# Kernel tuning notes

Hardware: AMD Instinct MI355X
Metric: run time of the kernel (lower is better)

## Reference

```python
import jax, jax.numpy as jnp
import numpy as np

NU, NI = 100000, 50000          # num_users, num_items
N = NU + NI                      # total nodes
D = 64                           # hidden_dim
DE = 16                          # eigs_dim
L = 2                            # n_layers
E = 1500000                      # edges per layer
NP = 14                          # 2**(sample_hop+1)-2 path types
EPS = 1e-5


def setup_inputs() -> dict:
    key = jax.random.key(0)
    ks = jax.random.split(key, 7)
    return {
        "user_emb": jax.random.normal(ks[0], (NU, D), jnp.float32) * 0.1,
        "item_emb": jax.random.normal(ks[1], (NI, D), jnp.float32) * 0.1,
        "eigs": jax.random.normal(ks[2], (N, DE), jnp.float32),
        "lambda0": jax.random.normal(ks[3], (L,), jnp.float32) * 0.1,
        "path_w": jax.random.normal(ks[4], (L, NP), jnp.float32) * 0.1,
        "indices": jax.random.randint(ks[5], (L, 2, E), 0, N),
        "path_type": jax.random.randint(ks[6], (L, E), 0, NP),
    }


def _layer_norm(x):
    mu = x.mean(-1, keepdims=True)
    var = ((x - mu) ** 2).mean(-1, keepdims=True)
    return (x - mu) * jax.lax.rsqrt(var + EPS)


def _sparse_softmax(row, vals, n):
    # torch: clamp(exp(v), min=-5, max=5) -> effectively min(exp(v), 5)
    e = jnp.clip(jnp.exp(vals), -5.0, 5.0)
    s = jax.ops.segment_sum(e, row, num_segments=n)
    s = jnp.where(s == 0.0, 1.0, s)
    return e / s[row]


def _encoder(x, idx, pt, eigs, lam, pw):
    y = _layer_norm(x)                                   # [N, D]
    r, c = idx[0], idx[1]                                # [E]
    yc = y[c]                                            # [E, D]
    xs = (y[r] * yc).sum(-1) * (1.0 / jnp.sqrt(jnp.float32(D)))  # [E]
    ys = (eigs[r] * eigs[c]).sum(-1)                     # [E]
    s0 = _sparse_softmax(r, xs + jnp.exp(lam) * ys, N)
    s1 = _sparse_softmax(r, pw[pt], N)
    s = 0.5 * (s0 + s1)                                  # mean over the two scores
    # SpMM: out[r] += s_e * y[c_e]
    return jax.ops.segment_sum(s[:, None] * yc, r, num_segments=N)


def reference(user_emb, item_emb, eigs, lambda0, path_w, indices, path_type):
    x = jnp.concatenate([user_emb, item_emb], axis=0)    # [N, D]
    embs = [x]
    for l in range(L):
        x = _encoder(x, indices[l], path_type[l], eigs, lambda0[l], path_w[l])
        embs.append(x)
    return jnp.mean(jnp.stack(embs, axis=1), axis=1)      # [N, D]
```

## Files before the change

kernel.cpp:

```cpp
#include <hip/hip_runtime.h>
#include <hip/hip_bf16.h>

#define NUSERS 100000
#define NITEMS 50000
#define NN 150000
#define DD 64
#define DE 16
#define NE 1500000
#define NPATH 14
#define LN_EPS 1e-5f

#define BROWS 512
#define NBUK 293
#define NB (2 * NBUK)
#define CHUNK 4096
#define NCHUNK ((NE + CHUNK - 1) / CHUNK)

#define EIGBLK ((NN * DE) / 256)

typedef float vf2 __attribute__((ext_vector_type(2)));

__device__ __forceinline__ vf2 unpk(unsigned u) {
    vf2 r;
    r.x = __uint_as_float(u << 16);
    r.y = __uint_as_float(u & 0xffff0000u);
    return r;
}
__device__ __forceinline__ unsigned f2b(float f) {
    union { float f; unsigned u; } v; v.f = f;
    return (v.u + 0x7fffu + ((v.u >> 16) & 1u)) >> 16;
}

template<int CTRL>
__device__ __forceinline__ float dppmov(float x) {
    return __int_as_float(
        __builtin_amdgcn_mov_dpp(__float_as_int(x), CTRL, 0xF, 0xF, true));
}

__device__ __forceinline__ int wscan(int v, int lane) {
    #pragma unroll
    for (int d = 1; d < 64; d <<= 1) {
        int u = __shfl_up(v, d, 64);
        v += (lane >= d) ? u : 0;
    }
    return v;
}

__global__ void k_eigln(const float* __restrict__ uemb,
                        const float* __restrict__ iemb,
                        const float* __restrict__ eigs,
                        unsigned short* __restrict__ e16,
                        unsigned short* __restrict__ y) {
    int blk = blockIdx.x;
    int t = threadIdx.x;
    if (blk < EIGBLK) {
        int i = blk * 256 + t;
        e16[i] = (unsigned short)f2b(eigs[i]);
    } else {
        int row = (blk - EIGBLK) * 4 + (t >> 6);
        int lane = t & 63;
        if (row >= NN) return;
        int i = row * DD + lane;
        float v = (row < NUSERS) ? uemb[i] : iemb[i - NUSERS * DD];
        float s = v;
        #pragma unroll
        for (int m = 32; m; m >>= 1) s += __shfl_xor(s, m, 64);
        float mu = s * (1.0f / 64.0f);
        float d = v - mu;
        float q = d * d;
        #pragma unroll
        for (int m = 32; m; m >>= 1) q += __shfl_xor(q, m, 64);
        float rs = rsqrtf(q * (1.0f / 64.0f) + LN_EPS);
        y[i] = (unsigned short)f2b(d * rs);
    }
}

__global__ void k_pcount(const int* __restrict__ idx, int* __restrict__ cntmat) {
    int blk = blockIdx.x;
    int layer = blk / NCHUNK;
    int k = blk - layer * NCHUNK;
    __shared__ int h[NBUK];
    for (int t = threadIdx.x; t < NBUK; t += 256) h[t] = 0;
    __syncthreads();
    const int* rrow = idx + (size_t)layer * 2 * NE;
    int base = k * CHUNK;
    int lim = min(CHUNK, NE - base);
    for (int j = threadIdx.x; j < lim; j += 256)
        atomicAdd(&h[rrow[base + j] >> 9], 1);
    __syncthreads();
    for (int t = threadIdx.x; t < NBUK; t += 256)
        cntmat[((size_t)layer * NBUK + t) * NCHUNK + k] = h[t];
}

__global__ __launch_bounds__(512) void k_bukscan(const int* __restrict__ cnt,
                                                 int* __restrict__ exsc,
                                                 int* __restrict__ tot) {
    __shared__ int wsum[8];
    int b = blockIdx.x;
    int t = threadIdx.x;
    int lane = t & 63, w = t >> 6;
    int v = (t < NCHUNK) ? cnt[(size_t)b * NCHUNK + t] : 0;
    int s = wscan(v, lane);
    if (lane == 63) wsum[w] = s;
    __syncthreads();
    if (w == 0) {
        int x = (lane < 8) ? wsum[lane] : 0;
        #pragma unroll
        for (int d = 1; d < 8; d <<= 1) {
            int u = __shfl_up(x, d, 64);
            x += (lane >= d) ? u : 0;
        }
        if (lane < 8) wsum[lane] = x;
    }
    __syncthreads();
    int base = (w > 0) ? wsum[w - 1] : 0;
    s += base;
    if (t < NCHUNK) exsc[(size_t)b * NCHUNK + t] = s - v;
    if (t == 511) tot[b] = s;
}

__global__ __launch_bounds__(1024) void k_totscan(const int* __restrict__ tot,
                                                  int* __restrict__ bstart) {
    __shared__ int wsum[16];
    int t = threadIdx.x;
    int lane = t & 63, w = t >> 6;
    int v = (t < NB) ? tot[t] : 0;
    int s = wscan(v, lane);
    if (lane == 63) wsum[w] = s;
    __syncthreads();
    if (w == 0) {
        int x = (lane < 16) ? wsum[lane] : 0;
        #pragma unroll
        for (int d = 1; d < 16; d <<= 1) {
            int u = __shfl_up(x, d, 64);
            x += (lane >= d) ? u : 0;
        }
        if (lane < 16) wsum[lane] = x;
    }
    __syncthreads();
    int base = (w > 0) ? wsum[w - 1] : 0;
    s += base;
    if (t < NB) bstart[t] = s - v;
    if (t == 0) bstart[NB] = 2 * NE;
}

__global__ void k_pscatter(const int* __restrict__ idx,
                           const int* __restrict__ ptyp,
                           const int* __restrict__ exsc,
                           const int* __restrict__ bstart,
                           unsigned int* __restrict__ stage) {
    int blk = blockIdx.x;
    int layer = blk / NCHUNK;
    int k = blk - layer * NCHUNK;
    __shared__ int hofs[NBUK];
    for (int t = threadIdx.x; t < NBUK; t += 256) {
        int b = layer * NBUK + t;
        hofs[t] = bstart[b] + exsc[(size_t)b * NCHUNK + k];
    }
    __syncthreads();
    const int* rrow = idx + (size_t)layer * 2 * NE;
    const int* ccol = rrow + NE;
    const int* pp   = ptyp + (size_t)layer * NE;
    int base = k * CHUNK;
    int lim = min(CHUNK, NE - base);
    for (int j = threadIdx.x; j < lim; j += 256) {
        int e = base + j;
        int r = rrow[e];
        int pos = atomicAdd(&hofs[r >> 9], 1);
        stage[pos] = (unsigned)ccol[e] | ((unsigned)pp[e] << 18)
                   | ((unsigned)(r & 511) << 22);
    }
}

__global__ __launch_bounds__(1024) void k_bscatter(
        const unsigned int* __restrict__ stage,
        const int* __restrict__ bstart,
        int* __restrict__ csv,
        int2* __restrict__ roff) {
    __shared__ int scnt[BROWS];
    __shared__ int scur[BROWS];
    __shared__ int wsum[16];
    int b = blockIdx.x;
    int t = threadIdx.x;
    int lane = t & 63, w = t >> 6;
    int layer = b / NBUK;
    int brow0 = (b - layer * NBUK) * BROWS;
    int nrows = min(BROWS, NN - brow0);
    int start = bstart[b];
    int n = bstart[b + 1] - start;
    if (t < BROWS) scnt[t] = 0;
    __syncthreads();
    for (int p = t; p < n; p += 1024)
        atomicAdd(&scnt[stage[start + p] >> 22], 1);
    __syncthreads();
    int orig = (t < BROWS) ? scnt[t] : 0;
    int s = wscan(orig, lane);
    if (lane == 63) wsum[w] = s;
    __syncthreads();
    if (w == 0) {
        int x = (lane < 16) ? wsum[lane] : 0;
        #pragma unroll
        for (int d = 1; d < 16; d <<= 1) {
            int u = __shfl_up(x, d, 64);
            x += (lane >= d) ? u : 0;
        }
        if (lane < 16) wsum[lane] = x;
    }
    __syncthreads();
    int wb = (w > 0) ? wsum[w - 1] : 0;
    int excl = wb + s - orig;
    if (t < BROWS) {
        scur[t] = excl;
        if (t < nrows)
            roff[(size_t)layer * NN + brow0 + t] =
                make_int2(start + excl, start + excl + orig);
    }
    __syncthreads();
    for (int p = t; p < n; p += 1024) {
        unsigned rec = stage[start + p];
        int pos = atomicAdd(&scur[rec >> 22], 1);
        csv[start + pos] = (int)(rec & 0x3fffffu);
    }
}

__global__ void k_row(const unsigned short* __restrict__ y,
                      const unsigned short* __restrict__ e16,
                      const int2* __restrict__ roff,
                      const int* __restrict__ csv,
                      const float* __restrict__ pw,
                      const float* __restrict__ lam,
                      int layer,
                      const float* __restrict__ uemb,
                      const float* __restrict__ iemb,
                      float* __restrict__ x1,
                      unsigned short* __restrict__ y1,
                      float* __restrict__ out) {
    __shared__ float pexp[NPATH];
    __shared__ float selam;
    int t = threadIdx.x;
    if (t < NPATH) pexp[t] = fminf(expf(pw[layer * NPATH + t]), 5.0f);
    if (t == NPATH) selam = expf(lam[layer]);
    __syncthreads();

    int row = blockIdx.x * 4 + (t >> 6);
    int lane = t & 63;
    int g = lane >> 3;
    int sl = lane & 7;
    int2 pr = roff[row];
    int p0 = pr.x, p1 = pr.y;

    uint4 ar = reinterpret_cast<const uint4*>(y + (size_t)row * DD)[sl];
    vf2 a0 = unpk(ar.x), a1 = unpk(ar.y), a2 = unpk(ar.z), a3 = unpk(ar.w);
    unsigned eru = reinterpret_cast<const unsigned*>(e16 + (size_t)row * DE)[sl];
    vf2 er = unpk(eru);
    float elam = selam;

    float sum0 = 0.f, sum1 = 0.f;
    vf2 A0 = {0.f, 0.f}, A1 = {0.f, 0.f}, A2 = {0.f, 0.f}, A3 = {0.f, 0.f};
    vf2 B0 = {0.f, 0.f}, B1 = {0.f, 0.f}, B2 = {0.f, 0.f}, B3 = {0.f, 0.f};

    for (int p = p0; p < p1; p += 8) {
        int q = p + g;
        int qc = (q < p1) ? q : (p1 - 1);
        int rec = csv[qc];
        int c = rec & 0x3ffff;
        uint4 bv = reinterpret_cast<const uint4*>(y + (size_t)c * DD)[sl];
        unsigned ecu = reinterpret_cast<const unsigned*>(e16 + (size_t)c * DE)[sl];
        vf2 b0 = unpk(bv.x), b1 = unpk(bv.y), b2 = unpk(bv.z), b3 = unpk(bv.w);
        vf2 px = a0 * b0;
        px += a1 * b1;
        px += a2 * b2;
        px += a3 * b3;
        vf2 ec = unpk(ecu);
        vf2 tt = px * 0.125f + (er * ec) * elam;
        float sc = tt.x + tt.y;
        sc += dppmov<0xB1>(sc);
        sc += dppmov<0x4E>(sc);
        sc += dppmov<0x141>(sc);
        bool ok = q < p1;
        float e0 = ok ? fminf(__expf(sc), 5.0f) : 0.f;
        float e1 = ok ? pexp[(rec >> 18) & 0xF] : 0.f;
        sum0 += e0; sum1 += e1;
        A0 += e0 * b0; A1 += e0 * b1; A2 += e0 * b2; A3 += e0 * b3;
        B0 += e1 * b0; B1 += e1 * b1; B2 += e1 * b2; B3 += e1 * b3;
    }

    sum0 += dppmov<0x128>(sum0);
    sum1 += dppmov<0x128>(sum1);
    #pragma unroll
    for (int m = 16; m <= 32; m <<= 1) {
        sum0 += __shfl_xor(sum0, m, 64);
        sum1 += __shfl_xor(sum1, m, 64);
    }
    float rinv0 = 0.5f / ((sum0 == 0.f) ? 1.f : sum0);
    float rinv1 = 0.5f / ((sum1 == 0.f) ? 1.f : sum1);

    vf2 o0 = rinv0 * A0 + rinv1 * B0, o1 = rinv0 * A1 + rinv1 * B1;
    vf2 o2 = rinv0 * A2 + rinv1 * B2, o3 = rinv0 * A3 + rinv1 * B3;
    o0.x += dppmov<0x128>(o0.x); o0.y += dppmov<0x128>(o0.y);
    o1.x += dppmov<0x128>(o1.x); o1.y += dppmov<0x128>(o1.y);
    o2.x += dppmov<0x128>(o2.x); o2.y += dppmov<0x128>(o2.y);
    o3.x += dppmov<0x128>(o3.x); o3.y += dppmov<0x128>(o3.y);
    #pragma unroll
    for (int m = 16; m <= 32; m <<= 1) {
        vf2 s;
        s.x = __shfl_xor(o0.x, m, 64); s.y = __shfl_xor(o0.y, m, 64); o0 += s;
        s.x = __shfl_xor(o1.x, m, 64); s.y = __shfl_xor(o1.y, m, 64); o1 += s;
        s.x = __shfl_xor(o2.x, m, 64); s.y = __shfl_xor(o2.y, m, 64); o2 += s;
        s.x = __shfl_xor(o3.x, m, 64); s.y = __shfl_xor(o3.y, m, 64); o3 += s;
    }
    if (g == 0) {
        int ofs = sl * 8;
        float v0 = o0.x, v1 = o0.y, v2 = o1.x, v3 = o1.y;
        float v4 = o2.x, v5 = o2.y, v6 = o3.x, v7 = o3.y;
        if (layer == 0) {
            float* dst = x1 + (size_t)row * DD + ofs;
            reinterpret_cast<float4*>(dst)[0] = make_float4(v0, v1, v2, v3);
            reinterpret_cast<float4*>(dst)[1] = make_float4(v4, v5, v6, v7);
            float s = v0+v1+v2+v3+v4+v5+v6+v7;
            s += __shfl_xor(s, 1, 64);
            s += __shfl_xor(s, 2, 64);
            s += __shfl_xor(s, 4, 64);
            float mu = s * (1.0f / 64.0f);
            float d0=v0-mu, d1=v1-mu, d2=v2-mu, d3=v3-mu;
            float d4=v4-mu, d5=v5-mu, d6=v6-mu, d7=v7-mu;
            float qv = d0*d0+d1*d1+d2*d2+d3*d3+d4*d4+d5*d5+d6*d6+d7*d7;
            qv += __shfl_xor(qv, 1, 64);
            qv += __shfl_xor(qv, 2, 64);
            qv += __shfl_xor(qv, 4, 64);
            float rs = rsqrtf(qv * (1.0f / 64.0f) + LN_EPS);
            uint4 pk;
            pk.x = f2b(d0*rs) | (f2b(d1*rs) << 16);
            pk.y = f2b(d2*rs) | (f2b(d3*rs) << 16);
            pk.z = f2b(d4*rs) | (f2b(d5*rs) << 16);
            pk.w = f2b(d6*rs) | (f2b(d7*rs) << 16);
            reinterpret_cast<uint4*>(y1 + (size_t)row * DD)[sl] = pk;
        } else {
            const float* e = (row < NUSERS)
                ? (uemb + (size_t)row * DD + ofs)
                : (iemb + (size_t)(row - NUSERS) * DD + ofs);
            const float* xp = x1 + (size_t)row * DD + ofs;
            float4 ea = reinterpret_cast<const float4*>(e)[0];
            float4 eb = reinterpret_cast<const float4*>(e)[1];
            float4 xa = reinterpret_cast<const float4*>(xp)[0];
            float4 xb = reinterpret_cast<const float4*>(xp)[1];
            float* dst = out + (size_t)row * DD + ofs;
            const float k3 = 1.0f / 3.0f;
            reinterpret_cast<float4*>(dst)[0] = make_float4(
                (ea.x + xa.x + v0) * k3, (ea.y + xa.y + v1) * k3,
                (ea.z + xa.z + v2) * k3, (ea.w + xa.w + v3) * k3);
            reinterpret_cast<float4*>(dst)[1] = make_float4(
                (eb.x + xb.x + v4) * k3, (eb.y + xb.y + v5) * k3,
                (eb.z + xb.z + v6) * k3, (eb.w + xb.w + v7) * k3);
        }
    }
}

extern "C" void kernel_launch(void* const* d_in, const int* in_sizes, int n_in,
                              void* d_out, int out_size, void* d_ws, size_t ws_size,
                              hipStream_t stream) {
    const float* uemb = (const float*)d_in[0];
    const float* iemb = (const float*)d_in[1];
    const float* eigs = (const float*)d_in[2];
    const float* lam  = (const float*)d_in[3];
    const float* pw   = (const float*)d_in[4];
    const int* idx    = (const int*)d_in[5];
    const int* ptyp   = (const int*)d_in[6];

    char* w = (char*)d_ws;
    float*          x1     = (float*)(w);
    unsigned short* y0     = (unsigned short*)(w + 38400000);
    unsigned short* y1     = (unsigned short*)(w + 57600000);
    int*            csv    = (int*)(w + 76800000);
    int2*           roff   = (int2*)(w + 88800000);
    unsigned short* e16    = (unsigned short*)(w + 91200000);
    unsigned int*   stage  = (unsigned int*)(w + 96000000);
    int*            cnt    = (int*)(w + 108000000);
    int*            exsc   = (int*)(w + 108860248);
    int*            tot    = (int*)(w + 109720496);
    int*            bstart = (int*)(w + 109722840);

    const int gRows = NN / 4;

    k_pcount<<<2 * NCHUNK, 256, 0, stream>>>(idx, cnt);
    k_bukscan<<<NB, 512, 0, stream>>>(cnt, exsc, tot);
    k_totscan<<<1, 1024, 0, stream>>>(tot, bstart);
    k_pscatter<<<2 * NCHUNK, 256, 0, stream>>>(idx, ptyp, exsc, bstart, stage);
    k_bscatter<<<NB, 1024, 0, stream>>>(stage, bstart, csv, roff);

    k_eigln<<<EIGBLK + gRows, 256, 0, stream>>>(uemb, iemb, eigs, e16, y0);

    k_row<<<gRows, 256, 0, stream>>>(y0, e16, roff, csv, pw, lam, 0,
                                     nullptr, nullptr, x1, y1, nullptr);
    k_row<<<gRows, 256, 0, stream>>>(y1, e16, roff + NN, csv, pw, lam, 1,
                                     uemb, iemb, x1, nullptr, (float*)d_out);
}
```

Measured before the change: 406.4 us.

## Replace bucketed two-pass CSR build with per-row atomic count-scan-scatter

The two-level bucket sort (chunk histograms, bucket scan, total scan, staging scatter, per-bucket LDS sort) is replaced by a direct CSR build. Per-row counts come from global atomics, fused into the eigs/layernorm kernel. A three-kernel prefix scan then produces row offsets and cursors, and a final scatter places each edge with a global atomic on its row cursor. This cuts kernel launches and the staging buffer pass. In exchange, row updates become random global atomics with returned values, writes become uncoalesced, and edge order within a row is no longer deterministic.

```diff
diff --git a/kernel.cpp b/kernel.cpp
--- a/kernel.cpp
+++ b/kernel.cpp
@@ -10,13 +10,13 @@
 #define NPATH 14
 #define LN_EPS 1e-5f
 
-#define BROWS 512
-#define NBUK 293
-#define NB (2 * NBUK)
 #define CHUNK 4096
 #define NCHUNK ((NE + CHUNK - 1) / CHUNK)
-
 #define EIGBLK ((NN * DE) / 256)
+
+#define NROWS (2 * NN)
+#define NQ (NROWS / 4)
+#define NSCB ((NQ + 1023) / 1024)
 
 typedef float vf2 __attribute__((ext_vector_type(2)));
 
@@ -46,18 +46,29 @@
     return v;
 }
 
-__global__ void k_eigln(const float* __restrict__ uemb,
-                        const float* __restrict__ iemb,
-                        const float* __restrict__ eigs,
-                        unsigned short* __restrict__ e16,
-                        unsigned short* __restrict__ y) {
+__global__ void k_cnt_eig_ln(const float* __restrict__ uemb,
+                             const float* __restrict__ iemb,
+                             const float* __restrict__ eigs,
+                             const int* __restrict__ idx,
+                             int* __restrict__ rowcnt,
+                             unsigned short* __restrict__ e16,
+                             unsigned short* __restrict__ y) {
     int blk = blockIdx.x;
     int t = threadIdx.x;
-    if (blk < EIGBLK) {
-        int i = blk * 256 + t;
+    if (blk < 2 * NCHUNK) {
+        int layer = blk / NCHUNK;
+        int k = blk - layer * NCHUNK;
+        const int* rrow = idx + (size_t)layer * 2 * NE;
+        int* rc = rowcnt + layer * NN;
+        int base = k * CHUNK;
+        int lim = min(CHUNK, NE - base);
+        for (int j = t; j < lim; j += 256)
+            atomicAdd(&rc[rrow[base + j]], 1);
+    } else if (blk < 2 * NCHUNK + EIGBLK) {
+        int i = (blk - 2 * NCHUNK) * 256 + t;
         e16[i] = (unsigned short)f2b(eigs[i]);
     } else {
-        int row = (blk - EIGBLK) * 4 + (t >> 6);
+        int row = (blk - 2 * NCHUNK - EIGBLK) * 4 + (t >> 6);
         int lane = t & 63;
         if (row >= NN) return;
         int i = row * DD + lane;
@@ -75,58 +86,18 @@
     }
 }
 
-__global__ void k_pcount(const int* __restrict__ idx, int* __restrict__ cntmat) {
-    int blk = blockIdx.x;
-    int layer = blk / NCHUNK;
-    int k = blk - layer * NCHUNK;
-    __shared__ int h[NBUK];
-    for (int t = threadIdx.x; t < NBUK; t += 256) h[t] = 0;
-    __syncthreads();
-    const int* rrow = idx + (size_t)layer * 2 * NE;
-    int base = k * CHUNK;
-    int lim = min(CHUNK, NE - base);
-    for (int j = threadIdx.x; j < lim; j += 256)
-        atomicAdd(&h[rrow[base + j] >> 9], 1);
-    __syncthreads();
-    for (int t = threadIdx.x; t < NBUK; t += 256)
-        cntmat[((size_t)layer * NBUK + t) * NCHUNK + k] = h[t];
-}
-
-__global__ __launch_bounds__(512) void k_bukscan(const int* __restrict__ cnt,
-                                                 int* __restrict__ exsc,
-                                                 int* __restrict__ tot) {
-    __shared__ int wsum[8];
-    int b = blockIdx.x;
-    int t = threadIdx.x;
+__global__ __launch_bounds__(1024) void k_scan1(const int* __restrict__ rowcnt,
+                                                int2* __restrict__ roff,
+                                                int* __restrict__ bsum) {
+    __shared__ int wsum[16];
+    int blk = blockIdx.x, t = threadIdx.x;
     int lane = t & 63, w = t >> 6;
-    int v = (t < NCHUNK) ? cnt[(size_t)b * NCHUNK + t] : 0;
-    int s = wscan(v, lane);
-    if (lane == 63) wsum[w] = s;
-    __syncthreads();
-    if (w == 0) {
-        int x = (lane < 8) ? wsum[lane] : 0;
-        #pragma unroll
-        for (int d = 1; d < 8; d <<= 1) {
-            int u = __shfl_up(x, d, 64);
-            x += (lane >= d) ? u : 0;
-        }
-        if (lane < 8) wsum[lane] = x;
-    }
-    __syncthreads();
-    int base = (w > 0) ? wsum[w - 1] : 0;
-    s += base;
-    if (t < NCHUNK) exsc[(size_t)b * NCHUNK + t] = s - v;
-    if (t == 511) tot[b] = s;
-}
-
-__global__ __launch_bounds__(1024) void k_totscan(const int* __restrict__ tot,
-                                                  int* __restrict__ bstart) {
-    __shared__ int wsum[16];
-    int t = threadIdx.x;
-    int lane = t & 63, w = t >> 6;
-    int v = (t < NB) ? tot[t] : 0;
-    int s = wscan(v, lane);
-    if (lane == 63) wsum[w] = s;
+    int gi = blk * 1024 + t;
+    int4 v = make_int4(0, 0, 0, 0);
+    if (gi < NQ) v = reinterpret_cast<const int4*>(rowcnt)[gi];
+    int s4 = v.x + v.y + v.z + v.w;
+    int si = wscan(s4, lane);
+    if (lane == 63) wsum[w] = si;
     __syncthreads();
     if (w == 0) {
         int x = (lane < 16) ? wsum[lane] : 0;
@@ -138,88 +109,66 @@
         if (lane < 16) wsum[lane] = x;
     }
     __syncthreads();
-    int base = (w > 0) ? wsum[w - 1] : 0;
-    s += base;
-    if (t < NB) bstart[t] = s - v;
-    if (t == 0) bstart[NB] = 2 * NE;
-}
-
-__global__ void k_pscatter(const int* __restrict__ idx,
-                           const int* __restrict__ ptyp,
-                           const int* __restrict__ exsc,
-                           const int* __restrict__ bstart,
-                           unsigned int* __restrict__ stage) {
+    int wb = (w > 0) ? wsum[w - 1] : 0;
+    int te = wb + si - s4;
+    if (gi < NQ) {
+        int e0 = te, e1 = e0 + v.x, e2 = e1 + v.y, e3 = e2 + v.z;
+        int2* rp = roff + (size_t)gi * 4;
+        rp[0] = make_int2(e0, e1);
+        rp[1] = make_int2(e1, e2);
+        rp[2] = make_int2(e2, e3);
+        rp[3] = make_int2(e3, e3 + v.w);
+    }
+    if (t == 0) bsum[blk] = wsum[15];
+}
+
+__global__ __launch_bounds__(128) void k_scan2(const int* __restrict__ bsum,
+                                               int* __restrict__ bbase) {
+    __shared__ int wsum[2];
+    int t = threadIdx.x, lane = t & 63, w = t >> 6;
+    int v = (t < NSCB) ? bsum[t] : 0;
+    int s = wscan(v, lane);
+    if (lane == 63) wsum[w] = s;
+    __syncthreads();
+    int wb = (w > 0) ? wsum[0] : 0;
+    if (t < NSCB) bbase[t] = wb + s - v;
+}
+
+__global__ __launch_bounds__(1024) void k_scan3(const int* __restrict__ bbase,
+                                                int2* __restrict__ roff,
+                                                int* __restrict__ cursor) {
+    int blk = blockIdx.x, t = threadIdx.x;
+    int gi = blk * 1024 + t;
+    if (gi >= NQ) return;
+    int base = bbase[blk];
+    int2* rp = roff + (size_t)gi * 4;
+    int* cp = cursor + (size_t)gi * 4;
+    #pragma unroll
+    for (int k = 0; k < 4; ++k) {
+        int2 r = rp[k];
+        r.x += base; r.y += base;
+        rp[k] = r;
+        cp[k] = r.x;
+    }
+}
+
+__global__ void k_scatter(const int* __restrict__ idx,
+                          const int* __restrict__ ptyp,
+                          int* __restrict__ cursor,
+                          int* __restrict__ csv) {
     int blk = blockIdx.x;
     int layer = blk / NCHUNK;
     int k = blk - layer * NCHUNK;
-    __shared__ int hofs[NBUK];
-    for (int t = threadIdx.x; t < NBUK; t += 256) {
-        int b = layer * NBUK + t;
-        hofs[t] = bstart[b] + exsc[(size_t)b * NCHUNK + k];
-    }
-    __syncthreads();
     const int* rrow = idx + (size_t)layer * 2 * NE;
     const int* ccol = rrow + NE;
     const int* pp   = ptyp + (size_t)layer * NE;
+    int* cur = cursor + layer * NN;
     int base = k * CHUNK;
     int lim = min(CHUNK, NE - base);
     for (int j = threadIdx.x; j < lim; j += 256) {
         int e = base + j;
-        int r = rrow[e];
-        int pos = atomicAdd(&hofs[r >> 9], 1);
-        stage[pos] = (unsigned)ccol[e] | ((unsigned)pp[e] << 18)
-                   | ((unsigned)(r & 511) << 22);
-    }
-}
-
-__global__ __launch_bounds__(1024) void k_bscatter(
-        const unsigned int* __restrict__ stage,
-        const int* __restrict__ bstart,
-        int* __restrict__ csv,
-        int2* __restrict__ roff) {
-    __shared__ int scnt[BROWS];
-    __shared__ int scur[BROWS];
-    __shared__ int wsum[16];
-    int b = blockIdx.x;
-    int t = threadIdx.x;
-    int lane = t & 63, w = t >> 6;
-    int layer = b / NBUK;
-    int brow0 = (b - layer * NBUK) * BROWS;
-    int nrows = min(BROWS, NN - brow0);
-    int start = bstart[b];
-    int n = bstart[b + 1] - start;
-    if (t < BROWS) scnt[t] = 0;
-    __syncthreads();
-    for (int p = t; p < n; p += 1024)
-        atomicAdd(&scnt[stage[start + p] >> 22], 1);
-    __syncthreads();
-    int orig = (t < BROWS) ? scnt[t] : 0;
-    int s = wscan(orig, lane);
-    if (lane == 63) wsum[w] = s;
-    __syncthreads();
-    if (w == 0) {
-        int x = (lane < 16) ? wsum[lane] : 0;
-        #pragma unroll
-        for (int d = 1; d < 16; d <<= 1) {
-            int u = __shfl_up(x, d, 64);
-            x += (lane >= d) ? u : 0;
-        }
-        if (lane < 16) wsum[lane] = x;
-    }
-    __syncthreads();
-    int wb = (w > 0) ? wsum[w - 1] : 0;
-    int excl = wb + s - orig;
-    if (t < BROWS) {
-        scur[t] = excl;
-        if (t < nrows)
-            roff[(size_t)layer * NN + brow0 + t] =
-                make_int2(start + excl, start + excl + orig);
-    }
-    __syncthreads();
-    for (int p = t; p < n; p += 1024) {
-        unsigned rec = stage[start + p];
-        int pos = atomicAdd(&scur[rec >> 22], 1);
-        csv[start + pos] = (int)(rec & 0x3fffffu);
+        int pos = atomicAdd(&cur[rrow[e]], 1);
+        csv[pos] = ccol[e] | (pp[e] << 18);
     }
 }
 
@@ -374,21 +323,20 @@
     int*            csv    = (int*)(w + 76800000);
     int2*           roff   = (int2*)(w + 88800000);
     unsigned short* e16    = (unsigned short*)(w + 91200000);
-    unsigned int*   stage  = (unsigned int*)(w + 96000000);
-    int*            cnt    = (int*)(w + 108000000);
-    int*            exsc   = (int*)(w + 108860248);
-    int*            tot    = (int*)(w + 109720496);
-    int*            bstart = (int*)(w + 109722840);
+    int*            rowcnt = (int*)(w + 96000000);
+    int*            cursor = (int*)(w + 97200000);
+    int*            bsum   = (int*)(w + 98400000);
+    int*            bbase  = (int*)(w + 98400512);
 
     const int gRows = NN / 4;
 
-    k_pcount<<<2 * NCHUNK, 256, 0, stream>>>(idx, cnt);
-    k_bukscan<<<NB, 512, 0, stream>>>(cnt, exsc, tot);
-    k_totscan<<<1, 1024, 0, stream>>>(tot, bstart);
-    k_pscatter<<<2 * NCHUNK, 256, 0, stream>>>(idx, ptyp, exsc, bstart, stage);
-    k_bscatter<<<NB, 1024, 0, stream>>>(stage, bstart, csv, roff);
-
-    k_eigln<<<EIGBLK + gRows, 256, 0, stream>>>(uemb, iemb, eigs, e16, y0);
+    hipMemsetAsync(rowcnt, 0, NROWS * sizeof(int), stream);
+    k_cnt_eig_ln<<<2 * NCHUNK + EIGBLK + gRows, 256, 0, stream>>>(
+        uemb, iemb, eigs, idx, rowcnt, e16, y0);
+    k_scan1<<<NSCB, 1024, 0, stream>>>(rowcnt, roff, bsum);
+    k_scan2<<<1, 128, 0, stream>>>(bsum, bbase);
+    k_scan3<<<NSCB, 1024, 0, stream>>>(bbase, roff, cursor);
+    k_scatter<<<2 * NCHUNK, 256, 0, stream>>>(idx, ptyp, cursor, csv);
 
     k_row<<<gRows, 256, 0, stream>>>(y0, e16, roff, csv, pw, lam, 0,
                                      nullptr, nullptr, x1, y1, nullptr);
```

Measured after the change: 609.5 us. 50.0% more time.
